# Kernel optimization log

Hardware: AMD Instinct MI355X
Metric: run time of the kernel (lower is better)

The kernel has to match this reference:

```python
import jax, jax.numpy as jnp
import numpy as np

jax.config.update("jax_enable_x64", True)  # hash math needs int64 (prime * coord > 2^31)

LEVEL = 16
MOD_T = 2 ** 16
FDIM = 3
_PRIMES = (1, 2654435761, 805459861)  # first feature_dim primes from the module


def _grid_sizes():
    # mirrors torch float32 computation: b = exp((log(n_max)-log(n_min))/(level-1))
    n_min = np.float32(4.0)
    n_max = np.float32(256.0)
    b = np.float32(np.exp((np.log(n_max) - np.log(n_min)) / np.float32(LEVEL - 1)))
    return [int(n_min * b ** i) for i in range(LEVEL)]


def setup_inputs() -> dict:
    key = jax.random.key(0)
    k1, k2 = jax.random.split(key)
    images = jax.random.uniform(k1, (16, 3, 256, 256), dtype=jnp.float32)
    hash_table = (jax.random.uniform(k2, (LEVEL, MOD_T, FDIM), dtype=jnp.float32)
                  * 0.0002 - 0.0001)
    return {"images": images, "hash_table": hash_table}


def reference(images, hash_table):
    b, c, h, w = images.shape
    primes = jnp.array(_PRIMES[:FDIM], dtype=jnp.int64)
    neg_inf = jnp.array(-jnp.inf, dtype=images.dtype)
    outs = []
    for lvl, grid in enumerate(_grid_sizes()):
        kh, kw = h // grid, w // grid
        # max_pool2d(images*grid, kernel=(kh,kw), stride=(kh,kw))
        pooled = jax.lax.reduce_window(
            images * grid, neg_inf, jax.lax.max,
            window_dimensions=(1, 1, kh, kw),
            window_strides=(1, 1, kh, kw),
            padding="VALID")                     # [B, F, gh, gw]
        idx = pooled.astype(jnp.int64) * primes[None, :, None, None]
        g = idx[:, 0]
        for i in range(1, FDIM):
            g = g ^ idx[:, i]
        g = g % MOD_T                             # [B, gh, gw]
        f = hash_table[lvl][g]                    # gather -> [B, gh, gw, F]
        f = jnp.transpose(f, (0, 3, 1, 2))        # [B, F, gh, gw]
        # F.interpolate(..., mode='bilinear') == half-pixel, align_corners=False
        f = jax.image.resize(f, (b, FDIM, h, w), method="bilinear")
        outs.append(f)
    return jnp.concatenate(outs, axis=1)          # [B, level*F, H, W]
```

## Files before the change

kernel.cpp:

```cpp
#include <hip/hip_runtime.h>
#include <stdint.h>
#include <math.h>


#define NLVL 16
#define NB   16

__constant__ int   c_P[NLVL]   = {4,5,6,9,12,15,21,28,36,51,64,85,128,256,256,256};
__constant__ float c_G[NLVL]   = {4.f,5.f,6.f,9.f,12.f,15.f,21.f,27.f,36.f,48.f,63.f,84.f,111.f,147.f,194.f,255.f};
__constant__ int   c_CUM[14]   = {0,16,41,77,158,302,527,968,1752,3048,5649,9745,16970,33354};

#define CELLS_PB   33354
#define CELLS_TOT  (CELLS_PB*NB)
#define MWS_FLOATS (CELLS_TOT*3)
#define POOL_BLOCKS (NB*32)
#define DIR_BLOCKS  1024
#define K1_BLOCKS   (POOL_BLOCKS + DIR_BLOCKS)
#define TILE_BLOCKS (13*16*16)

__device__ __forceinline__ uint32_t hash3(float m0, float m1, float m2, float g) {
    uint32_t v0 = (uint32_t)(int)(m0 * g);
    uint32_t v1 = (uint32_t)(int)(m1 * g);
    uint32_t v2 = (uint32_t)(int)(m2 * g);
    return (v0 ^ (v1 * 2654435761u) ^ (v2 * 805459861u)) & 0xFFFFu;
}

__global__ __launch_bounds__(256) void pool_direct(const float* __restrict__ img,
                                                   const float* __restrict__ tab,
                                                   unsigned int* __restrict__ mws,
                                                   float* __restrict__ out)
{
    static constexpr int K_P[13]   = {4,5,6,9,12,15,21,28,36,51,64,85,128};
    static constexpr int K_KH[13]  = {64,51,42,28,21,17,12,9,7,5,4,3,2};
    static constexpr int K_CUM[13] = {0,16,41,77,158,302,527,968,1752,3048,5649,9745,16970};

    __shared__ float simg[3][8][256];
    __shared__ float colbuf[3][256];

    if (blockIdx.x >= POOL_BLOCKS) {
        int t = (blockIdx.x - POOL_BLOCKS) * 256 + threadIdx.x;
        int b = t >> 14;
        int pix0 = (t & 16383) << 2;
        const float* p = img + (size_t)b * 196608 + pix0;
        float4 i0 = *(const float4*)p;
        float4 i1 = *(const float4*)(p + 65536);
        float4 i2 = *(const float4*)(p + 131072);
#pragma unroll
        for (int lvl = 13; lvl < 16; ++lvl) {
            float g = c_G[lvl];
            const float* T = tab + (size_t)lvl * 196608;
            uint32_t g0 = hash3(i0.x, i1.x, i2.x, g);
            uint32_t g1 = hash3(i0.y, i1.y, i2.y, g);
            uint32_t g2 = hash3(i0.z, i1.z, i2.z, g);
            uint32_t g3 = hash3(i0.w, i1.w, i2.w, g);
            float3 f0 = *(const float3*)(T + g0 * 3);
            float3 f1 = *(const float3*)(T + g1 * 3);
            float3 f2 = *(const float3*)(T + g2 * 3);
            float3 f3 = *(const float3*)(T + g3 * 3);
            float4 o0, o1, o2;
            o0.x = f0.x; o1.x = f0.y; o2.x = f0.z;
            o0.y = f1.x; o1.y = f1.y; o2.y = f1.z;
            o0.z = f2.x; o1.z = f2.y; o2.z = f2.z;
            o0.w = f3.x; o1.w = f3.y; o2.w = f3.z;
            float* ob = out + ((size_t)b * 48 + 3 * lvl) * 65536 + pix0;
            *(float4*)ob            = o0;
            *(float4*)(ob + 65536)  = o1;
            *(float4*)(ob + 131072) = o2;
        }
        return;
    }

    int b    = blockIdx.x >> 5;
    int band = blockIdx.x & 31;
    int y0   = band * 8;

    const float* base = img + (size_t)b * 196608 + (size_t)y0 * 256;
    for (int t = threadIdx.x; t < 1536; t += 256) {
        int ch = t >> 9;
        int r  = t & 511;
        float4 v = *(const float4*)(base + (size_t)ch * 65536 + r * 4);
        int row = r >> 6, c4 = (r & 63) << 2;
        simg[ch][row][c4 + 0] = v.x;
        simg[ch][row][c4 + 1] = v.y;
        simg[ch][row][c4 + 2] = v.z;
        simg[ch][row][c4 + 3] = v.w;
    }
    __syncthreads();

    int x = threadIdx.x;
#pragma unroll
    for (int lvl = 0; lvl < 13; ++lvl) {
        const int kh = K_KH[lvl], P = K_P[lvl];
        int nr0 = y0 / kh;
        int nr1 = (y0 + 7) / kh; if (nr1 > P - 1) nr1 = P - 1;
        for (int cr = nr0; cr <= nr1; ++cr) {
            int rlo = cr * kh;      if (rlo < y0) rlo = y0;
            int rhi = cr * kh + kh; if (rhi > y0 + 8) rhi = y0 + 8;
            float p0 = -INFINITY, p1 = -INFINITY, p2 = -INFINITY;
            for (int r = rlo; r < rhi; ++r) {
                int rr = r - y0;
                p0 = fmaxf(p0, simg[0][rr][x]);
                p1 = fmaxf(p1, simg[1][rr][x]);
                p2 = fmaxf(p2, simg[2][rr][x]);
            }
            colbuf[0][x] = p0; colbuf[1][x] = p1; colbuf[2][x] = p2;
            __syncthreads();
            if (x < P) {
                float q0 = -INFINITY, q1 = -INFINITY, q2 = -INFINITY;
                for (int c = x * kh; c < x * kh + kh; ++c) {
                    q0 = fmaxf(q0, colbuf[0][c]);
                    q1 = fmaxf(q1, colbuf[1][c]);
                    q2 = fmaxf(q2, colbuf[2][c]);
                }
                int idx = K_CUM[lvl] * NB + b * P * P + cr * P + x;
                atomicMax(&mws[idx],                 __float_as_uint(q0));
                atomicMax(&mws[idx + CELLS_TOT],     __float_as_uint(q1));
                atomicMax(&mws[idx + 2 * CELLS_TOT], __float_as_uint(q2));
            }
            __syncthreads();
        }
    }
}

__global__ __launch_bounds__(256) void render_tiles(const float* __restrict__ tab,
                                                    const float* __restrict__ mws,
                                                    float* __restrict__ out)
{
    __shared__ float4 s[34 * 34];
    int blk   = blockIdx.x;
    int tile  = blk & 15;
    int plane = blk >> 4;
    int lvl   = plane >> 4;
    int b     = plane & 15;
    int P     = c_P[lvl];
    int yt0   = (tile >> 2) * 64;
    int xt0   = (tile & 3) * 64;

    int nlo  = ((2 * yt0 + 1) * P - 256) >> 9;
    int r_lo = nlo < 0 ? 0 : (nlo > P - 1 ? P - 1 : nlo);
    int nhi  = (((2 * (yt0 + 63) + 1) * P - 256) >> 9) + 1;
    int r_hi = nhi < 0 ? 0 : (nhi > P - 1 ? P - 1 : nhi);
    int mlo  = ((2 * xt0 + 1) * P - 256) >> 9;
    int c_lo = mlo < 0 ? 0 : (mlo > P - 1 ? P - 1 : mlo);
    int mhi  = (((2 * (xt0 + 63) + 1) * P - 256) >> 9) + 1;
    int c_hi = mhi < 0 ? 0 : (mhi > P - 1 ? P - 1 : mhi);
    int span_y = r_hi - r_lo + 1;
    int span_x = c_hi - c_lo + 1;

    int planebase = c_CUM[lvl] * NB + b * P * P;
    const float* T = tab + (size_t)lvl * 196608;
    float gmul = c_G[lvl];
    int n = span_y * span_x;
    for (int t = threadIdx.x; t < n; t += 256) {
        int r = t / span_x, c = t - r * span_x;
        int idx = planebase + (r_lo + r) * P + c_lo + c;
        float m0 = mws[idx];
        float m1 = mws[idx + CELLS_TOT];
        float m2 = mws[idx + 2 * CELLS_TOT];
        uint32_t g = hash3(m0, m1, m2, gmul);
        float3 tv = *(const float3*)(T + g * 3);
        float4 fv; fv.x = tv.x; fv.y = tv.y; fv.z = tv.z; fv.w = 0.f;
        s[t] = fv;
    }
    __syncthreads();

    int lane = threadIdx.x & 63;
    int w    = threadIdx.x >> 6;
    int xq   = lane & 15;
    int rg   = lane >> 4;
    int xb   = xt0 + xq * 4;

    int ix0t[4], ix1t[4]; float wx0t[4], wx1t[4];
#pragma unroll
    for (int j = 0; j < 4; ++j) {
        int numx = (2 * (xb + j) + 1) * P - 256;
        int ix0  = numx >> 9;
        float fx = (float)(numx & 511) * (1.0f / 512.0f);
        int ix1;
        if (ix0 < 0)           { ix0 = 0;     ix1 = 0;     fx = 0.f; }
        else if (ix0 >= P - 1) { ix0 = P - 1; ix1 = P - 1; fx = 0.f; }
        else                   { ix1 = ix0 + 1; }
        ix0t[j] = ix0 - c_lo; ix1t[j] = ix1 - c_lo; wx1t[j] = fx; wx0t[j] = 1.f - fx;
    }

    int cur0 = -1, cur1 = -1;
    float r0v[3][4], r1v[3][4];

#pragma unroll
    for (int k = 0; k < 4; ++k) {
        int y = yt0 + w * 16 + rg * 4 + k;
        int numy = (2 * y + 1) * P - 256;
        int iy0  = numy >> 9;
        float fy = (float)(numy & 511) * (1.0f / 512.0f);
        int iy1;
        if (iy0 < 0)           { iy0 = 0;     iy1 = 0;     fy = 0.f; }
        else if (iy0 >= P - 1) { iy0 = P - 1; iy1 = P - 1; fy = 0.f; }
        else                   { iy1 = iy0 + 1; }

        if (iy0 != cur0) {
            if (iy0 == cur1) {
#pragma unroll
                for (int j = 0; j < 4; ++j) {
                    r0v[0][j] = r1v[0][j]; r0v[1][j] = r1v[1][j]; r0v[2][j] = r1v[2][j];
                }
            } else {
                const float4* p0 = s + (iy0 - r_lo) * span_x;
#pragma unroll
                for (int j = 0; j < 4; ++j) {
                    float4 a = p0[ix0t[j]], q = p0[ix1t[j]];
                    r0v[0][j] = wx0t[j] * a.x + wx1t[j] * q.x;
                    r0v[1][j] = wx0t[j] * a.y + wx1t[j] * q.y;
                    r0v[2][j] = wx0t[j] * a.z + wx1t[j] * q.z;
                }
            }
            cur0 = iy0;
        }
        if (iy1 != cur1) {
            if (iy1 == cur0 && iy1 == iy0) {
#pragma unroll
                for (int j = 0; j < 4; ++j) {
                    r1v[0][j] = r0v[0][j]; r1v[1][j] = r0v[1][j]; r1v[2][j] = r0v[2][j];
                }
            } else {
                const float4* p1 = s + (iy1 - r_lo) * span_x;
#pragma unroll
                for (int j = 0; j < 4; ++j) {
                    float4 a = p1[ix0t[j]], q = p1[ix1t[j]];
                    r1v[0][j] = wx0t[j] * a.x + wx1t[j] * q.x;
                    r1v[1][j] = wx0t[j] * a.y + wx1t[j] * q.y;
                    r1v[2][j] = wx0t[j] * a.z + wx1t[j] * q.z;
                }
            }
            cur1 = iy1;
        }

        float wy1 = fy, wy0 = 1.f - fy;
        float* o = out + ((size_t)b * 48 + 3 * lvl) * 65536 + (size_t)y * 256 + xb;
#pragma unroll
        for (int c = 0; c < 3; ++c) {
            float4 q;
            q.x = wy0 * r0v[c][0] + wy1 * r1v[c][0];
            q.y = wy0 * r0v[c][1] + wy1 * r1v[c][1];
            q.z = wy0 * r0v[c][2] + wy1 * r1v[c][2];
            q.w = wy0 * r0v[c][3] + wy1 * r1v[c][3];
            *(float4*)(o + (size_t)c * 65536) = q;
        }
    }
}

extern "C" void kernel_launch(void* const* d_in, const int* in_sizes, int n_in,
                              void* d_out, int out_size, void* d_ws, size_t ws_size,
                              hipStream_t stream)
{
    const float* img = (const float*)d_in[0];
    const float* tab = (const float*)d_in[1];
    float* out = (float*)d_out;
    float* mws = (float*)d_ws;

    (void)hipMemsetAsync(mws, 0, (size_t)MWS_FLOATS * sizeof(float), stream);
    hipLaunchKernelGGL(pool_direct,  dim3(K1_BLOCKS), dim3(256), 0, stream, img, tab, (unsigned int*)mws, out);
    hipLaunchKernelGGL(render_tiles, dim3(TILE_BLOCKS), dim3(256), 0, stream, tab, mws, out);
}
```

Measured before the change: 74.97 us.

## Assign one wavefront per pooled cell-row, drop atomics and workspace memset

```diff
diff --git a/kernel.cpp b/kernel.cpp
--- a/kernel.cpp
+++ b/kernel.cpp
@@ -12,8 +12,8 @@
 
 #define CELLS_PB   33354
 #define CELLS_TOT  (CELLS_PB*NB)
-#define MWS_FLOATS (CELLS_TOT*3)
-#define POOL_BLOCKS (NB*32)
+#define TASKS_TOT  7424
+#define POOL_BLOCKS (TASKS_TOT/4)
 #define DIR_BLOCKS  1024
 #define K1_BLOCKS   (POOL_BLOCKS + DIR_BLOCKS)
 #define TILE_BLOCKS (13*16*16)
@@ -25,17 +25,24 @@
     return (v0 ^ (v1 * 2654435761u) ^ (v2 * 805459861u)) & 0xFFFFu;
 }
 
+__device__ __forceinline__ float4 max4(float4 a, float4 b) {
+    float4 r;
+    r.x = fmaxf(a.x, b.x); r.y = fmaxf(a.y, b.y);
+    r.z = fmaxf(a.z, b.z); r.w = fmaxf(a.w, b.w);
+    return r;
+}
+
 __global__ __launch_bounds__(256) void pool_direct(const float* __restrict__ img,
                                                    const float* __restrict__ tab,
-                                                   unsigned int* __restrict__ mws,
+                                                   float* __restrict__ mws,
                                                    float* __restrict__ out)
 {
-    static constexpr int K_P[13]   = {4,5,6,9,12,15,21,28,36,51,64,85,128};
-    static constexpr int K_KH[13]  = {64,51,42,28,21,17,12,9,7,5,4,3,2};
-    static constexpr int K_CUM[13] = {0,16,41,77,158,302,527,968,1752,3048,5649,9745,16970};
-
-    __shared__ float simg[3][8][256];
-    __shared__ float colbuf[3][256];
+    static constexpr int K_P[13]     = {4,5,6,9,12,15,21,28,36,51,64,85,128};
+    static constexpr int K_KH[13]    = {64,51,42,28,21,17,12,9,7,5,4,3,2};
+    static constexpr int K_CUM[13]   = {0,16,41,77,158,302,527,968,1752,3048,5649,9745,16970};
+    static constexpr int K_ROW16[13] = {0,64,144,240,384,576,816,1152,1600,2176,2992,4016,5376};
+
+    __shared__ float4 sw[4][3][64];
 
     if (blockIdx.x >= POOL_BLOCKS) {
         int t = (blockIdx.x - POOL_BLOCKS) * 256 + threadIdx.x;
@@ -70,55 +77,46 @@
         return;
     }
 
-    int b    = blockIdx.x >> 5;
-    int band = blockIdx.x & 31;
-    int y0   = band * 8;
-
-    const float* base = img + (size_t)b * 196608 + (size_t)y0 * 256;
-    for (int t = threadIdx.x; t < 1536; t += 256) {
-        int ch = t >> 9;
-        int r  = t & 511;
-        float4 v = *(const float4*)(base + (size_t)ch * 65536 + r * 4);
-        int row = r >> 6, c4 = (r & 63) << 2;
-        simg[ch][row][c4 + 0] = v.x;
-        simg[ch][row][c4 + 1] = v.y;
-        simg[ch][row][c4 + 2] = v.z;
-        simg[ch][row][c4 + 3] = v.w;
-    }
+    int wid  = threadIdx.x >> 6;
+    int lane = threadIdx.x & 63;
+    int task = (blockIdx.x << 2) + wid;
+
+    int lvl = 0;
+#pragma unroll
+    for (int l = 1; l < 13; ++l) lvl += (task >= K_ROW16[l]);
+    int P = K_P[lvl], kh = K_KH[lvl];
+    int rem = task - K_ROW16[lvl];
+    int b   = rem / P;
+    int cr  = rem - b * P;
+
+    const float4* rp = (const float4*)(img + (size_t)b * 196608) + (size_t)(cr * kh) * 64 + lane;
+    float4 cm0 = make_float4(-INFINITY, -INFINITY, -INFINITY, -INFINITY);
+    float4 cm1 = cm0, cm2 = cm0;
+    for (int r = 0; r < kh; ++r, rp += 64) {
+        cm0 = max4(cm0, rp[0]);
+        cm1 = max4(cm1, rp[16384]);
+        cm2 = max4(cm2, rp[32768]);
+    }
+    sw[wid][0][lane] = cm0;
+    sw[wid][1][lane] = cm1;
+    sw[wid][2][lane] = cm2;
     __syncthreads();
 
-    int x = threadIdx.x;
-#pragma unroll
-    for (int lvl = 0; lvl < 13; ++lvl) {
-        const int kh = K_KH[lvl], P = K_P[lvl];
-        int nr0 = y0 / kh;
-        int nr1 = (y0 + 7) / kh; if (nr1 > P - 1) nr1 = P - 1;
-        for (int cr = nr0; cr <= nr1; ++cr) {
-            int rlo = cr * kh;      if (rlo < y0) rlo = y0;
-            int rhi = cr * kh + kh; if (rhi > y0 + 8) rhi = y0 + 8;
-            float p0 = -INFINITY, p1 = -INFINITY, p2 = -INFINITY;
-            for (int r = rlo; r < rhi; ++r) {
-                int rr = r - y0;
-                p0 = fmaxf(p0, simg[0][rr][x]);
-                p1 = fmaxf(p1, simg[1][rr][x]);
-                p2 = fmaxf(p2, simg[2][rr][x]);
-            }
-            colbuf[0][x] = p0; colbuf[1][x] = p1; colbuf[2][x] = p2;
-            __syncthreads();
-            if (x < P) {
-                float q0 = -INFINITY, q1 = -INFINITY, q2 = -INFINITY;
-                for (int c = x * kh; c < x * kh + kh; ++c) {
-                    q0 = fmaxf(q0, colbuf[0][c]);
-                    q1 = fmaxf(q1, colbuf[1][c]);
-                    q2 = fmaxf(q2, colbuf[2][c]);
-                }
-                int idx = K_CUM[lvl] * NB + b * P * P + cr * P + x;
-                atomicMax(&mws[idx],                 __float_as_uint(q0));
-                atomicMax(&mws[idx + CELLS_TOT],     __float_as_uint(q1));
-                atomicMax(&mws[idx + 2 * CELLS_TOT], __float_as_uint(q2));
-            }
-            __syncthreads();
-        }
+    const float* f0 = (const float*)&sw[wid][0][0];
+    const float* f1 = (const float*)&sw[wid][1][0];
+    const float* f2 = (const float*)&sw[wid][2][0];
+    for (int cx = lane; cx < P; cx += 64) {
+        float m0 = -INFINITY, m1 = -INFINITY, m2 = -INFINITY;
+        int cb = cx * kh;
+        for (int c = cb; c < cb + kh; ++c) {
+            m0 = fmaxf(m0, f0[c]);
+            m1 = fmaxf(m1, f1[c]);
+            m2 = fmaxf(m2, f2[c]);
+        }
+        int idx = K_CUM[lvl] * NB + b * P * P + cr * P + cx;
+        mws[idx]                 = m0;
+        mws[idx + CELLS_TOT]     = m1;
+        mws[idx + 2 * CELLS_TOT] = m2;
     }
 }
 
@@ -257,7 +255,6 @@
     float* out = (float*)d_out;
     float* mws = (float*)d_ws;
 
-    (void)hipMemsetAsync(mws, 0, (size_t)MWS_FLOATS * sizeof(float), stream);
-    hipLaunchKernelGGL(pool_direct,  dim3(K1_BLOCKS), dim3(256), 0, stream, img, tab, (unsigned int*)mws, out);
+    hipLaunchKernelGGL(pool_direct,  dim3(K1_BLOCKS), dim3(256), 0, stream, img, tab, mws, out);
     hipLaunchKernelGGL(render_tiles, dim3(TILE_BLOCKS), dim3(256), 0, stream, tab, mws, out);
 }
```

After: 89.73 us. 1.2x slower.
